# Performance work log

Measured on AMD Instinct MI355X. Metric: run time of the kernel, lower is better.

## Reference

```python
import jax, jax.numpy as jnp
import numpy as np

THRESHOLD_IOU = 0.8  # forward default in the original module


def setup_inputs() -> dict:
    key = jax.random.key(0)
    k1, k2, k3, k4 = jax.random.split(key, 4)
    N = M = 16
    H = W = 768
    # Binary masks (the original zeroes pixels to 0.0 and tests >0 via torch.where)
    masks_a = (jax.random.uniform(k1, (N, H, W)) > 0.6).astype(jnp.float32)
    masks_b = (jax.random.uniform(k2, (M, H, W)) > 0.6).astype(jnp.float32)
    # Make a few masks identical across labels so the IoU>threshold (suppression)
    # branch is exercised, not just the partial-overlap zeroing branch.
    masks_b = masks_b.at[:4].set(masks_a[:4])
    scores_a = jax.random.uniform(k3, (N,))
    scores_b = jax.random.uniform(k4, (M,))
    return {"masks_a": masks_a, "masks_b": masks_b,
            "scores_a": scores_a, "scores_b": scores_b}


def _overlap_filter(masks_a, masks_b, scores_a, scores_b, thr):
    # Sequential pairwise IoU + overlap zeroing, faithful to the original
    # nested product(enumerate(masks), enumerate(other_masks)) loop order
    # (i outer, j inner), where each pair sees masks already modified by
    # earlier pairs. Pruning ("keep") is applied after the loop; here it is
    # represented with static shapes as keep flags + zeroed-out rows.
    N, H, W = masks_a.shape
    M = masks_b.shape[0]
    P = H * W
    A0 = masks_a.reshape(N, P)
    B0 = masks_b.reshape(M, P)

    def body(carry, k):
        A, B, fi, fj = carry
        i = k // M
        j = k % M
        a = A[i]  # [P]
        b = B[j]  # [P]
        abin = a > 0
        bbin = b > 0
        inter = abin & bbin
        inter_sum = jnp.sum(inter.astype(jnp.float32))
        union_sum = jnp.sum((abin | bbin).astype(jnp.float32))
        iou = inter_sum / jnp.maximum(union_sum, 1.0)
        a_wins = scores_a[i] > scores_b[j]
        suppress = iou > thr                 # mark whole loser mask for removal
        zero_case = (iou > 0) & ~suppress    # zero overlapped pixels of loser
        b_new = jnp.where(zero_case & a_wins & inter, 0.0, b)
        a_new = jnp.where(zero_case & (~a_wins) & inter, 0.0, a)
        A = A.at[i].set(a_new)
        B = B.at[j].set(b_new)
        fj = fj.at[j].set(fj[j] | (suppress & a_wins))
        fi = fi.at[i].set(fi[i] | (suppress & ~a_wins))
        return (A, B, fi, fj), None

    fi0 = jnp.zeros(N, dtype=bool)
    fj0 = jnp.zeros(M, dtype=bool)
    (A, B, fi, fj), _ = jax.lax.scan(body, (A0, B0, fi0, fj0), jnp.arange(N * M))
    keep_a = ~fi
    keep_b = ~fj
    A = jnp.where(keep_a[:, None], A, 0.0)
    B = jnp.where(keep_b[:, None], B, 0.0)
    return A.reshape(N, H, W), B.reshape(M, H, W), keep_a, keep_b


def reference(masks_a, masks_b, scores_a, scores_b):
    return _overlap_filter(masks_a, masks_b, scores_a, scores_b, THRESHOLD_IOU)
```

## Files before the change

kernel.cpp:

```cpp
#include <hip/hip_runtime.h>
#include <stdint.h>

#define NM 16
#define HW_P 589824
#define WPM 18432
#define U8PM 9216
#define F4PM 147456
#define F4PT 2359296
#define PT 512
#define NG 8
#define U8PT 18

typedef unsigned long long u64;


__device__ __forceinline__ uint32_t spread4(uint32_t x) {
    uint32_t t = (x | (x << 12)) & 0x000F000Fu;
    t = (t | (t << 6)) & 0x03030303u;
    t = (t | (t << 3)) & 0x11111111u;
    return t;
}

__global__ __launch_bounds__(256) void binarize_kernel(
    const float* __restrict__ ma, const float* __restrict__ mb,
    uint32_t* __restrict__ bitsA, uint32_t* __restrict__ bitsB)
{
    int g = blockIdx.x * 256 + threadIdx.x;
    int tensor = (g >= F4PT);
    int lg = tensor ? (g - F4PT) : g;
    const float* src = tensor ? mb : ma;
    float4 v = ((const float4*)src)[lg];
    unsigned long long q0 = __ballot(v.x > 0.0f);
    unsigned long long q1 = __ballot(v.y > 0.0f);
    unsigned long long q2 = __ballot(v.z > 0.0f);
    unsigned long long q3 = __ballot(v.w > 0.0f);
    int lane = threadIdx.x & 63;
    if (lane < 8) {
        uint32_t wd = spread4((uint32_t)(q0 >> (8 * lane)) & 0xFFu)
                    | (spread4((uint32_t)(q1 >> (8 * lane)) & 0xFFu) << 1)
                    | (spread4((uint32_t)(q2 >> (8 * lane)) & 0xFFu) << 2)
                    | (spread4((uint32_t)(q3 >> (8 * lane)) & 0xFFu) << 3);
        uint32_t* bits = tensor ? bitsB : bitsA;
        bits[((lg & ~63) >> 3) + lane] = wd;
    }
}

__global__ __launch_bounds__(PT, 2) void pipeline_kernel(
    const float* __restrict__ sa, const float* __restrict__ sb,
    uint32_t* bitsA, uint32_t* bitsB, int* meta, u64* msg)
{
    int* flagsA = meta + 32;
    int* flagsB = meta + 48;
    unsigned* cons = (unsigned*)(meta + 64);
    unsigned* prodflag = (unsigned*)(meta + 96);

    const int g = blockIdx.x;
    const int tid = threadIdx.x;
    const int wave = tid >> 6, lane = tid & 63;
    const int c0 = 2 * g, c1 = 2 * g + 1;

    __shared__ int part[2][8][4];
    __shared__ unsigned smeta_s;

    u64* A8 = (u64*)bitsA;
    u64* B8 = (u64*)bitsB;

    u64 a[U8PT], b0[U8PT], b1[U8PT];
    int par = 0;

    int v0 = 0, v1 = 0;
#pragma unroll
    for (int w = 0; w < U8PT; ++w) {
        b0[w] = B8[(size_t)c0 * U8PM + tid + PT * w];
        b1[w] = B8[(size_t)c1 * U8PM + tid + PT * w];
        v0 += __popcll(b0[w]);
        v1 += __popcll(b1[w]);
    }
#pragma unroll
    for (int off = 32; off >= 1; off >>= 1) {
        v0 += __shfl_xor(v0, off); v1 += __shfl_xor(v1, off);
    }
    if (lane == 0) { part[par][wave][0] = v0; part[par][wave][1] = v1; }
    __syncthreads();
    int pcb0 = 0, pcb1 = 0;
#pragma unroll
    for (int w = 0; w < 8; ++w) { pcb0 += part[par][w][0]; pcb1 += part[par][w][1]; }
    par ^= 1;
    float sb0 = sb[c0], sb1 = sb[c1];
    int fb0 = 0, fb1 = 0;

    for (int t = 0; t < NM; ++t) {
        if (g > 0 && tid == 0) {
            unsigned v;
            while (!(v = __hip_atomic_load(&prodflag[(g - 1) * 16 + t],
                                           __ATOMIC_RELAXED, __HIP_MEMORY_SCOPE_AGENT)))
                __builtin_amdgcn_s_sleep(1);
            smeta_s = v;
        }
        if (g < NG - 1 && t >= 2 && tid == 64) {
            while (__hip_atomic_load(&cons[g], __ATOMIC_RELAXED,
                                     __HIP_MEMORY_SCOPE_AGENT) < (unsigned)(t - 1))
                __builtin_amdgcn_s_sleep(1);
        }
        __syncthreads();

        int pca, fa;
        if (g == 0) {
#pragma unroll
            for (int w = 0; w < U8PT; ++w)
                a[w] = A8[(size_t)t * U8PM + tid + PT * w];
            fa = 0; pca = 0;
        } else {
            unsigned v = smeta_s;
            pca = (int)((v >> 1) & 0xFFFFFu);
            fa  = (int)((v >> 21) & 1u);
            const u64* slot_in = msg + (size_t)((g - 1) * 2 + (t & 1)) * U8PM;
#pragma unroll
            for (int w = 0; w < U8PT; ++w)
                a[w] = __hip_atomic_load(&slot_in[tid + PT * w],
                                         __ATOMIC_RELAXED, __HIP_MEMORY_SCOPE_AGENT);
        }

        int i0 = 0, i1 = 0, it = 0, ip = 0;
#pragma unroll
        for (int w = 0; w < U8PT; ++w) {
            u64 ab0 = a[w] & b0[w];
            i0 += __popcll(ab0);
            i1 += __popcll(a[w] & b1[w]);
            it += __popcll(ab0 & b1[w]);
        }
        if (g == 0) {
#pragma unroll
            for (int w = 0; w < U8PT; ++w) ip += __popcll(a[w]);
        }
#pragma unroll
        for (int off = 32; off >= 1; off >>= 1) {
            i0 += __shfl_xor(i0, off); i1 += __shfl_xor(i1, off);
            it += __shfl_xor(it, off); ip += __shfl_xor(ip, off);
        }
        if (lane == 0) {
            part[par][wave][0] = i0; part[par][wave][1] = i1;
            part[par][wave][2] = it; part[par][wave][3] = ip;
        }
        __syncthreads();
        if (g > 0 && tid == 65)
            __hip_atomic_store(&cons[g - 1], (unsigned)(t + 1),
                               __ATOMIC_RELAXED, __HIP_MEMORY_SCOPE_AGENT);
        int I0 = 0, I1 = 0, T = 0, PC = 0;
#pragma unroll
        for (int w = 0; w < 8; ++w) {
            I0 += part[par][w][0]; I1 += part[par][w][1];
            T  += part[par][w][2]; PC += part[par][w][3];
        }
        par ^= 1;
        if (g == 0) pca = PC;

        float sai = sa[t];
        bool aupd = false;
        {
            int inter = I0;
            int uni = pca + pcb0 - inter;
            float iou = (float)inter / fmaxf((float)uni, 1.0f);
            bool aw = sai > sb0;
            if (iou > 0.8f) { if (aw) fb0 = 1; else fa = 1; }
            else if (inter > 0) {
                if (aw) {
                    pcb0 -= inter;
#pragma unroll
                    for (int w = 0; w < U8PT; ++w) b0[w] &= ~a[w];
                } else {
                    pca -= inter; aupd = true;
#pragma unroll
                    for (int w = 0; w < U8PT; ++w) a[w] &= ~b0[w];
                }
            }
        }
        {
            int inter = aupd ? (I1 - T) : I1;
            int uni = pca + pcb1 - inter;
            float iou = (float)inter / fmaxf((float)uni, 1.0f);
            bool aw = sai > sb1;
            if (iou > 0.8f) { if (aw) fb1 = 1; else fa = 1; }
            else if (inter > 0) {
                if (aw) {
                    pcb1 -= inter;
#pragma unroll
                    for (int w = 0; w < U8PT; ++w) b1[w] &= ~a[w];
                } else {
                    pca -= inter;
#pragma unroll
                    for (int w = 0; w < U8PT; ++w) a[w] &= ~b1[w];
                }
            }
        }

        if (g < NG - 1) {
            u64* slot_out = msg + (size_t)(g * 2 + (t & 1)) * U8PM;
#pragma unroll
            for (int w = 0; w < U8PT; ++w)
                __hip_atomic_store(&slot_out[tid + PT * w], a[w],
                                   __ATOMIC_RELAXED, __HIP_MEMORY_SCOPE_AGENT);
            __syncthreads();
            if (tid == 0)
                __hip_atomic_store(&prodflag[g * 16 + t],
                                   1u | ((unsigned)pca << 1) | ((unsigned)fa << 21),
                                   __ATOMIC_RELAXED, __HIP_MEMORY_SCOPE_AGENT);
        } else {
#pragma unroll
            for (int w = 0; w < U8PT; ++w)
                A8[(size_t)t * U8PM + tid + PT * w] = a[w];
            if (tid == 0) flagsA[t] = fa;
        }
    }
#pragma unroll
    for (int w = 0; w < U8PT; ++w) {
        B8[(size_t)c0 * U8PM + tid + PT * w] = b0[w];
        B8[(size_t)c1 * U8PM + tid + PT * w] = b1[w];
    }
    if (tid == 0) { flagsB[c0] = fb0; flagsB[c1] = fb1; }
}

__global__ __launch_bounds__(256) void expand_kernel(
    const uint32_t* __restrict__ bitsA, const uint32_t* __restrict__ bitsB,
    const int* __restrict__ meta, float* __restrict__ out)
{
    int g = blockIdx.x * 256 + threadIdx.x;
    int tensor = (g >= F4PT);
    int lg = tensor ? (g - F4PT) : g;
    const uint32_t* bits = tensor ? bitsB : bitsA;
    const int* flags = meta + (tensor ? 48 : 32);
    int m = lg / F4PM;
    bool keep = (flags[m] == 0);
    uint32_t wd = keep ? bits[lg >> 3] : 0u;
    int sh = (lg & 7) * 4;
    float4 o;
    o.x = ((wd >> (sh + 0)) & 1u) ? 1.0f : 0.0f;
    o.y = ((wd >> (sh + 1)) & 1u) ? 1.0f : 0.0f;
    o.z = ((wd >> (sh + 2)) & 1u) ? 1.0f : 0.0f;
    o.w = ((wd >> (sh + 3)) & 1u) ? 1.0f : 0.0f;
    ((float4*)out)[g] = o;
    if (g < 2 * NM) {
        const int* f = meta + 32;
        out[(size_t)2 * NM * HW_P + g] = f[g] ? 0.0f : 1.0f;
    }
}

extern "C" void kernel_launch(void* const* d_in, const int* in_sizes, int n_in,
                              void* d_out, int out_size, void* d_ws, size_t ws_size,
                              hipStream_t stream)
{
    const float* ma = (const float*)d_in[0];
    const float* mb = (const float*)d_in[1];
    const float* sa = (const float*)d_in[2];
    const float* sb = (const float*)d_in[3];
    float* out = (float*)d_out;
    char* ws = (char*)d_ws;

    uint32_t* bitsA = (uint32_t*)(ws);
    uint32_t* bitsB = (uint32_t*)(ws + 1179648);
    int* meta       = (int*)(ws + 2359296);
    u64* msg        = (u64*)(ws + 2360320);

    hipMemsetAsync(meta + 64, 0, 576, stream);

    binarize_kernel<<<18432, 256, 0, stream>>>(ma, mb, bitsA, bitsB);
    pipeline_kernel<<<NG, PT, 0, stream>>>(sa, sb, bitsA, bitsB, meta, msg);
    expand_kernel<<<18432, 256, 0, stream>>>(bitsA, bitsB, meta, out);
}
```

Before: 252.1 us.

## Replace 8-block mask pipeline with 72-workgroup pixel-split filter using global count reductions

The sequential filter is restructured from an 8-block chain, which passed the whole A mask between blocks, into 72 single-wave workgroups that each own a slice of pixels for all 32 masks. For each 2x2 tile of (i,j) pairs, every workgroup computes nine partial popcounts covering the combinations needed to correct intersections after earlier zeroing. These are published to flag-tagged global slots, and each workgroup spins until all 72 have posted before deciding the pair outcomes identically. Slot zeroing moves into the binarize kernel in place of a memset, and loads and stores use nontemporal hints. This spreads the bit work across many CUs but adds 64 grid-wide all-to-all exchanges and relies on all 72 workgroups being co-resident.

```diff
diff --git a/kernel.cpp b/kernel.cpp
--- a/kernel.cpp
+++ b/kernel.cpp
@@ -3,16 +3,22 @@
 
 #define NM 16
 #define HW_P 589824
-#define WPM 18432
 #define U8PM 9216
 #define F4PM 147456
 #define F4PT 2359296
-#define PT 512
-#define NG 8
-#define U8PT 18
+#define NWG 72
+#define SLOT0 864
+#define SLOTB 154368
 
 typedef unsigned long long u64;
-
+typedef float vf4 __attribute__((ext_vector_type(4)));
+
+__device__ __forceinline__ u64 aload64(const u64* p) {
+    return __hip_atomic_load(p, __ATOMIC_RELAXED, __HIP_MEMORY_SCOPE_AGENT);
+}
+__device__ __forceinline__ void astore64(u64* p, u64 v) {
+    __hip_atomic_store(p, v, __ATOMIC_RELAXED, __HIP_MEMORY_SCOPE_AGENT);
+}
 
 __device__ __forceinline__ uint32_t spread4(uint32_t x) {
     uint32_t t = (x | (x << 12)) & 0x000F000Fu;
@@ -23,17 +29,22 @@
 
 __global__ __launch_bounds__(256) void binarize_kernel(
     const float* __restrict__ ma, const float* __restrict__ mb,
-    uint32_t* __restrict__ bitsA, uint32_t* __restrict__ bitsB)
+    uint32_t* __restrict__ bitsA, uint32_t* __restrict__ bitsB,
+    uint4* __restrict__ slots4)
 {
+    if (blockIdx.x < 38) {
+        int idx = blockIdx.x * 256 + threadIdx.x;
+        if (idx < SLOTB / 16) { uint4 z = {0u,0u,0u,0u}; slots4[idx] = z; }
+    }
     int g = blockIdx.x * 256 + threadIdx.x;
     int tensor = (g >= F4PT);
     int lg = tensor ? (g - F4PT) : g;
     const float* src = tensor ? mb : ma;
-    float4 v = ((const float4*)src)[lg];
-    unsigned long long q0 = __ballot(v.x > 0.0f);
-    unsigned long long q1 = __ballot(v.y > 0.0f);
-    unsigned long long q2 = __ballot(v.z > 0.0f);
-    unsigned long long q3 = __ballot(v.w > 0.0f);
+    vf4 v = __builtin_nontemporal_load(((const vf4*)src) + lg);
+    u64 q0 = __ballot(v.x > 0.0f);
+    u64 q1 = __ballot(v.y > 0.0f);
+    u64 q2 = __ballot(v.z > 0.0f);
+    u64 q3 = __ballot(v.w > 0.0f);
     int lane = threadIdx.x & 63;
     if (lane < 8) {
         uint32_t wd = spread4((uint32_t)(q0 >> (8 * lane)) & 0xFFu)
@@ -45,179 +56,271 @@
     }
 }
 
-__global__ __launch_bounds__(PT, 2) void pipeline_kernel(
+__global__ __launch_bounds__(64, 1) void filter_kernel(
     const float* __restrict__ sa, const float* __restrict__ sb,
-    uint32_t* bitsA, uint32_t* bitsB, int* meta, u64* msg)
+    uint32_t* bitsA, uint32_t* bitsB, int* meta, u64* slots)
 {
-    int* flagsA = meta + 32;
-    int* flagsB = meta + 48;
-    unsigned* cons = (unsigned*)(meta + 64);
-    unsigned* prodflag = (unsigned*)(meta + 96);
-
-    const int g = blockIdx.x;
-    const int tid = threadIdx.x;
-    const int wave = tid >> 6, lane = tid & 63;
-    const int c0 = 2 * g, c1 = 2 * g + 1;
-
-    __shared__ int part[2][8][4];
-    __shared__ unsigned smeta_s;
-
+    const int wg = blockIdx.x;
+    const int lane = threadIdx.x;
     u64* A8 = (u64*)bitsA;
     u64* B8 = (u64*)bitsB;
-
-    u64 a[U8PT], b0[U8PT], b1[U8PT];
-    int par = 0;
-
-    int v0 = 0, v1 = 0;
-#pragma unroll
-    for (int w = 0; w < U8PT; ++w) {
-        b0[w] = B8[(size_t)c0 * U8PM + tid + PT * w];
-        b1[w] = B8[(size_t)c1 * U8PM + tid + PT * w];
-        v0 += __popcll(b0[w]);
-        v1 += __popcll(b1[w]);
-    }
-#pragma unroll
-    for (int off = 32; off >= 1; off >>= 1) {
-        v0 += __shfl_xor(v0, off); v1 += __shfl_xor(v1, off);
-    }
-    if (lane == 0) { part[par][wave][0] = v0; part[par][wave][1] = v1; }
+    const size_t base = (size_t)wg * 128 + lane;
+
+    __shared__ u64 ALds[16][128];
+    __shared__ int s_pcA[16];
+
+    u64 pk[11];
+#pragma unroll
+    for (int i = 0; i < 11; ++i) pk[i] = 0;
+    for (int m = 0; m < 16; ++m) {
+        u64 x0 = A8[(size_t)m * U8PM + base];
+        u64 x1 = A8[(size_t)m * U8PM + base + 64];
+        ALds[m][lane] = x0; ALds[m][64 + lane] = x1;
+        int c = __popcll(x0) + __popcll(x1);
+        pk[m / 3] += (u64)c << ((m % 3) * 16);
+    }
+    u64 B[16][2];
+#pragma unroll
+    for (int m = 0; m < 16; ++m) {
+        B[m][0] = B8[(size_t)m * U8PM + base];
+        B[m][1] = B8[(size_t)m * U8PM + base + 64];
+        int c = __popcll(B[m][0]) + __popcll(B[m][1]);
+        int mm = 16 + m;
+        pk[mm / 3] += (u64)c << ((mm % 3) * 16);
+    }
+#pragma unroll
+    for (int off = 32; off >= 1; off >>= 1)
+#pragma unroll
+        for (int i = 0; i < 11; ++i) pk[i] += __shfl_xor(pk[i], off);
+
+    u64* myinit = slots + (size_t)wg * 12;
+    if (lane == 0) {
+#pragma unroll
+        for (int i = 0; i < 11; ++i) astore64(&myinit[i], pk[i] | (1ull << 63));
+    }
+    asm volatile("" ::: "memory");
+    int pcw[32];
+    {
+        u64 v[11], v2[11];
+        const u64* s1 = slots + (size_t)lane * 12;
+        const u64* s2 = slots + (size_t)(64 + lane) * 12;
+        const bool two = (lane < 8);
+        bool okall;
+        do {
+            bool ok = true;
+#pragma unroll
+            for (int i = 0; i < 11; ++i) { v[i] = aload64(&s1[i]); ok &= (v[i] >> 63) != 0; }
+            if (two) {
+#pragma unroll
+                for (int i = 0; i < 11; ++i) { v2[i] = aload64(&s2[i]); ok &= (v2[i] >> 63) != 0; }
+            }
+            okall = __all(ok);
+        } while (!okall);
+#pragma unroll
+        for (int m = 0; m < 32; ++m) {
+            int f = (int)((v[m / 3] >> ((m % 3) * 16)) & 0xFFFF);
+            if (two) f += (int)((v2[m / 3] >> ((m % 3) * 16)) & 0xFFFF);
+            pcw[m] = f;
+        }
+        u64 q[11];
+#pragma unroll
+        for (int i = 0; i < 11; ++i) q[i] = 0;
+#pragma unroll
+        for (int m = 0; m < 32; ++m) q[m / 3] += (u64)pcw[m] << ((m % 3) * 21);
+#pragma unroll
+        for (int off = 32; off >= 1; off >>= 1)
+#pragma unroll
+            for (int i = 0; i < 11; ++i) q[i] += __shfl_xor(q[i], off);
+#pragma unroll
+        for (int m = 0; m < 32; ++m)
+            pcw[m] = (int)((q[m / 3] >> ((m % 3) * 21)) & 0x1FFFFF);
+    }
+    if (lane == 0) {
+#pragma unroll
+        for (int m = 0; m < 16; ++m) s_pcA[m] = pcw[m];
+    }
     __syncthreads();
-    int pcb0 = 0, pcb1 = 0;
-#pragma unroll
-    for (int w = 0; w < 8; ++w) { pcb0 += part[par][w][0]; pcb1 += part[par][w][1]; }
-    par ^= 1;
-    float sb0 = sb[c0], sb1 = sb[c1];
-    int fb0 = 0, fb1 = 0;
-
-    for (int t = 0; t < NM; ++t) {
-        if (g > 0 && tid == 0) {
-            unsigned v;
-            while (!(v = __hip_atomic_load(&prodflag[(g - 1) * 16 + t],
-                                           __ATOMIC_RELAXED, __HIP_MEMORY_SCOPE_AGENT)))
-                __builtin_amdgcn_s_sleep(1);
-            smeta_s = v;
+
+    int pcb[16];
+    float sBr[16];
+#pragma unroll
+    for (int j = 0; j < 16; ++j) { pcb[j] = pcw[16 + j]; sBr[j] = sb[j]; }
+    unsigned faM = 0, fbM = 0;
+
+    for (int rt = 0; rt < 8; ++rt) {
+        const int i0 = 2 * rt, i1 = i0 + 1;
+        u64 a0[2], a1[2];
+        a0[0] = ALds[i0][lane]; a0[1] = ALds[i0][64 + lane];
+        a1[0] = ALds[i1][lane]; a1[1] = ALds[i1][64 + lane];
+        int pca0 = s_pcA[i0], pca1 = s_pcA[i1];
+        int fa0 = 0, fa1 = 0;
+        float sa0 = sa[i0], sa1 = sa[i1];
+
+#pragma unroll
+        for (int ct = 0; ct < 8; ++ct) {
+            const int j0 = 2 * ct, j1 = j0 + 1;
+            const int k = rt * 8 + ct;
+            int t9[9];
+            {
+                int s0=0,s1=0,s2=0,s3=0,s4=0,s5=0,s6=0,s7=0,s8=0;
+#pragma unroll
+                for (int w = 0; w < 2; ++w) {
+                    u64 A0 = a0[w], A1 = a1[w], B0 = B[j0][w], B1 = B[j1][w];
+                    u64 ab  = A0 & B0;
+                    u64 ab1 = A0 & B1;
+                    u64 cb  = A1 & B0;
+                    u64 cb1 = A1 & B1;
+                    s0 += __popcll(ab);
+                    s1 += __popcll(ab1);
+                    s2 += __popcll(ab & B1);
+                    s3 += __popcll(cb);
+                    s4 += __popcll(cb & A0);
+                    s5 += __popcll(cb1);
+                    s6 += __popcll(cb1 & A0);
+                    s7 += __popcll(cb1 & B0);
+                    s8 += __popcll(cb1 & B0 & A0);
+                }
+                t9[0]=s0; t9[1]=s1; t9[2]=s2; t9[3]=s3; t9[4]=s4;
+                t9[5]=s5; t9[6]=s6; t9[7]=s7; t9[8]=s8;
+            }
+            u64 w0 = (u64)t9[0] | ((u64)t9[1] << 16) | ((u64)t9[2] << 32);
+            u64 w1 = (u64)t9[3] | ((u64)t9[4] << 16) | ((u64)t9[5] << 32);
+            u64 w2 = (u64)t9[6] | ((u64)t9[7] << 16) | ((u64)t9[8] << 32);
+#pragma unroll
+            for (int off = 32; off >= 1; off >>= 1) {
+                w0 += __shfl_xor(w0, off);
+                w1 += __shfl_xor(w1, off);
+                w2 += __shfl_xor(w2, off);
+            }
+            u64* ss = slots + SLOT0 + ((size_t)k * NWG + wg) * 4;
+            if (lane == 0) {
+                astore64(&ss[0], w0 | (1ull << 63));
+                astore64(&ss[1], w1 | (1ull << 63));
+                astore64(&ss[2], w2 | (1ull << 63));
+            }
+            asm volatile("" ::: "memory");
+            int T[9];
+            {
+                const u64* g1 = slots + SLOT0 + ((size_t)k * NWG + lane) * 4;
+                const u64* g2 = slots + SLOT0 + ((size_t)k * NWG + 64 + lane) * 4;
+                const bool two = (lane < 8);
+                u64 x0, x1, x2, y0 = 0, y1 = 0, y2 = 0;
+                bool okall;
+                do {
+                    x0 = aload64(&g1[0]); x1 = aload64(&g1[1]); x2 = aload64(&g1[2]);
+                    bool ok = ((x0 & x1 & x2) >> 63) != 0;
+                    if (two) {
+                        y0 = aload64(&g2[0]); y1 = aload64(&g2[1]); y2 = aload64(&g2[2]);
+                        ok &= ((y0 & y1 & y2) >> 63) != 0;
+                    }
+                    okall = __all(ok);
+                } while (!okall);
+                u64 q0 = 0, q1 = 0, q2 = 0;
+#pragma unroll
+                for (int f = 0; f < 3; ++f) {
+                    q0 += (u64)((x0 >> (f * 16)) & 0xFFFF) << (f * 21);
+                    q1 += (u64)((x1 >> (f * 16)) & 0xFFFF) << (f * 21);
+                    q2 += (u64)((x2 >> (f * 16)) & 0xFFFF) << (f * 21);
+                    if (two) {
+                        q0 += (u64)((y0 >> (f * 16)) & 0xFFFF) << (f * 21);
+                        q1 += (u64)((y1 >> (f * 16)) & 0xFFFF) << (f * 21);
+                        q2 += (u64)((y2 >> (f * 16)) & 0xFFFF) << (f * 21);
+                    }
+                }
+#pragma unroll
+                for (int off = 32; off >= 1; off >>= 1) {
+                    q0 += __shfl_xor(q0, off);
+                    q1 += __shfl_xor(q1, off);
+                    q2 += __shfl_xor(q2, off);
+                }
+#pragma unroll
+                for (int f = 0; f < 3; ++f) {
+                    T[f]     = (int)((q0 >> (f * 21)) & 0x1FFFFF);
+                    T[3 + f] = (int)((q1 >> (f * 21)) & 0x1FFFFF);
+                    T[6 + f] = (int)((q2 >> (f * 21)) & 0x1FFFFF);
+                }
+            }
+            bool a0l = false, b0l = false, b1l = false, a1l = false;
+            {
+                int inter = T[0];
+                int uni = pca0 + pcb[j0] - inter;
+                float iou = (float)inter / fmaxf((float)uni, 1.0f);
+                bool aw = sa0 > sBr[j0];
+                if (iou > 0.8f) { if (aw) fbM |= 1u << j0; else fa0 = 1; }
+                else if (inter > 0) {
+                    if (aw) { pcb[j0] -= inter; b0l = true;
+                              B[j0][0] &= ~a0[0]; B[j0][1] &= ~a0[1]; }
+                    else    { pca0 -= inter; a0l = true;
+                              a0[0] &= ~B[j0][0]; a0[1] &= ~B[j0][1]; }
+                }
+            }
+            {
+                int inter = T[1] - (a0l ? T[2] : 0);
+                int uni = pca0 + pcb[j1] - inter;
+                float iou = (float)inter / fmaxf((float)uni, 1.0f);
+                bool aw = sa0 > sBr[j1];
+                if (iou > 0.8f) { if (aw) fbM |= 1u << j1; else fa0 = 1; }
+                else if (inter > 0) {
+                    if (aw) { pcb[j1] -= inter; b1l = true;
+                              B[j1][0] &= ~a0[0]; B[j1][1] &= ~a0[1]; }
+                    else    { pca0 -= inter;
+                              a0[0] &= ~B[j1][0]; a0[1] &= ~B[j1][1]; }
+                }
+            }
+            {
+                int inter = T[3] - (b0l ? T[4] : 0);
+                int uni = pca1 + pcb[j0] - inter;
+                float iou = (float)inter / fmaxf((float)uni, 1.0f);
+                bool aw = sa1 > sBr[j0];
+                if (iou > 0.8f) { if (aw) fbM |= 1u << j0; else fa1 = 1; }
+                else if (inter > 0) {
+                    if (aw) { pcb[j0] -= inter;
+                              B[j0][0] &= ~a1[0]; B[j0][1] &= ~a1[1]; }
+                    else    { pca1 -= inter; a1l = true;
+                              a1[0] &= ~B[j0][0]; a1[1] &= ~B[j0][1]; }
+                }
+            }
+            {
+                int termA = T[5] - (b1l ? (T[6] - (a0l ? T[8] : 0)) : 0);
+                int inter = termA;
+                if (a1l) {
+                    int termB = (T[7] - (b0l ? T[8] : 0))
+                              - ((b1l && !a0l && !b0l) ? T[8] : 0);
+                    inter = termA - termB;
+                }
+                int uni = pca1 + pcb[j1] - inter;
+                float iou = (float)inter / fmaxf((float)uni, 1.0f);
+                bool aw = sa1 > sBr[j1];
+                if (iou > 0.8f) { if (aw) fbM |= 1u << j1; else fa1 = 1; }
+                else if (inter > 0) {
+                    if (aw) { pcb[j1] -= inter;
+                              B[j1][0] &= ~a1[0]; B[j1][1] &= ~a1[1]; }
+                    else    { pca1 -= inter;
+                              a1[0] &= ~B[j1][0]; a1[1] &= ~B[j1][1]; }
+                }
+            }
         }
-        if (g < NG - 1 && t >= 2 && tid == 64) {
-            while (__hip_atomic_load(&cons[g], __ATOMIC_RELAXED,
-                                     __HIP_MEMORY_SCOPE_AGENT) < (unsigned)(t - 1))
-                __builtin_amdgcn_s_sleep(1);
+        ALds[i0][lane] = a0[0]; ALds[i0][64 + lane] = a0[1];
+        ALds[i1][lane] = a1[0]; ALds[i1][64 + lane] = a1[1];
+        faM |= ((unsigned)fa0 << i0) | ((unsigned)fa1 << i1);
+    }
+
+    for (int m = 0; m < 16; ++m) {
+        A8[(size_t)m * U8PM + base]      = ALds[m][lane];
+        A8[(size_t)m * U8PM + base + 64] = ALds[m][64 + lane];
+    }
+#pragma unroll
+    for (int m = 0; m < 16; ++m) {
+        B8[(size_t)m * U8PM + base]      = B[m][0];
+        B8[(size_t)m * U8PM + base + 64] = B[m][1];
+    }
+    if (wg == 0 && lane == 0) {
+#pragma unroll
+        for (int m = 0; m < 16; ++m) {
+            meta[16 + m] = (int)((faM >> m) & 1u);
+            meta[32 + m] = (int)((fbM >> m) & 1u);
         }
-        __syncthreads();
-
-        int pca, fa;
-        if (g == 0) {
-#pragma unroll
-            for (int w = 0; w < U8PT; ++w)
-                a[w] = A8[(size_t)t * U8PM + tid + PT * w];
-            fa = 0; pca = 0;
-        } else {
-            unsigned v = smeta_s;
-            pca = (int)((v >> 1) & 0xFFFFFu);
-            fa  = (int)((v >> 21) & 1u);
-            const u64* slot_in = msg + (size_t)((g - 1) * 2 + (t & 1)) * U8PM;
-#pragma unroll
-            for (int w = 0; w < U8PT; ++w)
-                a[w] = __hip_atomic_load(&slot_in[tid + PT * w],
-                                         __ATOMIC_RELAXED, __HIP_MEMORY_SCOPE_AGENT);
-        }
-
-        int i0 = 0, i1 = 0, it = 0, ip = 0;
-#pragma unroll
-        for (int w = 0; w < U8PT; ++w) {
-            u64 ab0 = a[w] & b0[w];
-            i0 += __popcll(ab0);
-            i1 += __popcll(a[w] & b1[w]);
-            it += __popcll(ab0 & b1[w]);
-        }
-        if (g == 0) {
-#pragma unroll
-            for (int w = 0; w < U8PT; ++w) ip += __popcll(a[w]);
-        }
-#pragma unroll
-        for (int off = 32; off >= 1; off >>= 1) {
-            i0 += __shfl_xor(i0, off); i1 += __shfl_xor(i1, off);
-            it += __shfl_xor(it, off); ip += __shfl_xor(ip, off);
-        }
-        if (lane == 0) {
-            part[par][wave][0] = i0; part[par][wave][1] = i1;
-            part[par][wave][2] = it; part[par][wave][3] = ip;
-        }
-        __syncthreads();
-        if (g > 0 && tid == 65)
-            __hip_atomic_store(&cons[g - 1], (unsigned)(t + 1),
-                               __ATOMIC_RELAXED, __HIP_MEMORY_SCOPE_AGENT);
-        int I0 = 0, I1 = 0, T = 0, PC = 0;
-#pragma unroll
-        for (int w = 0; w < 8; ++w) {
-            I0 += part[par][w][0]; I1 += part[par][w][1];
-            T  += part[par][w][2]; PC += part[par][w][3];
-        }
-        par ^= 1;
-        if (g == 0) pca = PC;
-
-        float sai = sa[t];
-        bool aupd = false;
-        {
-            int inter = I0;
-            int uni = pca + pcb0 - inter;
-            float iou = (float)inter / fmaxf((float)uni, 1.0f);
-            bool aw = sai > sb0;
-            if (iou > 0.8f) { if (aw) fb0 = 1; else fa = 1; }
-            else if (inter > 0) {
-                if (aw) {
-                    pcb0 -= inter;
-#pragma unroll
-                    for (int w = 0; w < U8PT; ++w) b0[w] &= ~a[w];
-                } else {
-                    pca -= inter; aupd = true;
-#pragma unroll
-                    for (int w = 0; w < U8PT; ++w) a[w] &= ~b0[w];
-                }
-            }
-        }
-        {
-            int inter = aupd ? (I1 - T) : I1;
-            int uni = pca + pcb1 - inter;
-            float iou = (float)inter / fmaxf((float)uni, 1.0f);
-            bool aw = sai > sb1;
-            if (iou > 0.8f) { if (aw) fb1 = 1; else fa = 1; }
-            else if (inter > 0) {
-                if (aw) {
-                    pcb1 -= inter;
-#pragma unroll
-                    for (int w = 0; w < U8PT; ++w) b1[w] &= ~a[w];
-                } else {
-                    pca -= inter;
-#pragma unroll
-                    for (int w = 0; w < U8PT; ++w) a[w] &= ~b1[w];
-                }
-            }
-        }
-
-        if (g < NG - 1) {
-            u64* slot_out = msg + (size_t)(g * 2 + (t & 1)) * U8PM;
-#pragma unroll
-            for (int w = 0; w < U8PT; ++w)
-                __hip_atomic_store(&slot_out[tid + PT * w], a[w],
-                                   __ATOMIC_RELAXED, __HIP_MEMORY_SCOPE_AGENT);
-            __syncthreads();
-            if (tid == 0)
-                __hip_atomic_store(&prodflag[g * 16 + t],
-                                   1u | ((unsigned)pca << 1) | ((unsigned)fa << 21),
-                                   __ATOMIC_RELAXED, __HIP_MEMORY_SCOPE_AGENT);
-        } else {
-#pragma unroll
-            for (int w = 0; w < U8PT; ++w)
-                A8[(size_t)t * U8PM + tid + PT * w] = a[w];
-            if (tid == 0) flagsA[t] = fa;
-        }
-    }
-#pragma unroll
-    for (int w = 0; w < U8PT; ++w) {
-        B8[(size_t)c0 * U8PM + tid + PT * w] = b0[w];
-        B8[(size_t)c1 * U8PM + tid + PT * w] = b1[w];
-    }
-    if (tid == 0) { flagsB[c0] = fb0; flagsB[c1] = fb1; }
+    }
 }
 
 __global__ __launch_bounds__(256) void expand_kernel(
@@ -228,20 +331,19 @@
     int tensor = (g >= F4PT);
     int lg = tensor ? (g - F4PT) : g;
     const uint32_t* bits = tensor ? bitsB : bitsA;
-    const int* flags = meta + (tensor ? 48 : 32);
+    const int* flags = meta + (tensor ? 32 : 16);
     int m = lg / F4PM;
     bool keep = (flags[m] == 0);
     uint32_t wd = keep ? bits[lg >> 3] : 0u;
     int sh = (lg & 7) * 4;
-    float4 o;
+    vf4 o;
     o.x = ((wd >> (sh + 0)) & 1u) ? 1.0f : 0.0f;
     o.y = ((wd >> (sh + 1)) & 1u) ? 1.0f : 0.0f;
     o.z = ((wd >> (sh + 2)) & 1u) ? 1.0f : 0.0f;
     o.w = ((wd >> (sh + 3)) & 1u) ? 1.0f : 0.0f;
-    ((float4*)out)[g] = o;
+    __builtin_nontemporal_store(o, ((vf4*)out) + g);
     if (g < 2 * NM) {
-        const int* f = meta + 32;
-        out[(size_t)2 * NM * HW_P + g] = f[g] ? 0.0f : 1.0f;
+        out[(size_t)2 * NM * HW_P + g] = meta[16 + g] ? 0.0f : 1.0f;
     }
 }
 
@@ -259,11 +361,10 @@
     uint32_t* bitsA = (uint32_t*)(ws);
     uint32_t* bitsB = (uint32_t*)(ws + 1179648);
     int* meta       = (int*)(ws + 2359296);
-    u64* msg        = (u64*)(ws + 2360320);
-
-    hipMemsetAsync(meta + 64, 0, 576, stream);
-
-    binarize_kernel<<<18432, 256, 0, stream>>>(ma, mb, bitsA, bitsB);
-    pipeline_kernel<<<NG, PT, 0, stream>>>(sa, sb, bitsA, bitsB, meta, msg);
+    u64* slots      = (u64*)(ws + 2363392);
+
+    binarize_kernel<<<18432, 256, 0, stream>>>(ma, mb, bitsA, bitsB,
+                                               (uint4*)(ws + 2363392));
+    filter_kernel<<<NWG, 64, 0, stream>>>(sa, sb, bitsA, bitsB, meta, slots);
     expand_kernel<<<18432, 256, 0, stream>>>(bitsA, bitsB, meta, out);
 }
```

Measured after the change: 377.0 us. +49.5%, slower.
